# Kernel optimization log

Measured on AMD Instinct MI355X. Metric: run time of the kernel, lower is better.

Reference implementation:

```python
import jax, jax.numpy as jnp
import numpy as np

ALPHA = 0.02
NEG = -9e15

def lrelu(x):
    return jnp.where(x >= 0, x, ALPHA * x)

def layer_norm(x, eps=1e-5):
    m = jnp.mean(x, axis=-1, keepdims=True)
    v = jnp.var(x, axis=-1, keepdims=True)
    return (x - m) * jax.lax.rsqrt(v + eps)

def setup_inputs() -> dict:
    key = jax.random.key(0)
    ks = jax.random.split(key, 10)
    B, N, F_IN, D = 8, 2048, 10, 128
    h = jax.random.normal(ks[0], (B, N, F_IN), jnp.float32)
    adj = jax.random.randint(ks[1], (B, N, N), 0, 2, jnp.int32)
    s = 0.1
    return {
        "h": h,
        "adj": adj,
        "W1": jax.random.normal(ks[2], (D, F_IN), jnp.float32) * s,
        "b1": jax.random.normal(ks[3], (D,), jnp.float32) * s,
        "Wg": jax.random.normal(ks[4], (D, D), jnp.float32) * s,
        "bg": jax.random.normal(ks[5], (D,), jnp.float32) * s,
        "a1": jax.random.normal(ks[6], (D,), jnp.float32) * s,
        "a2": jax.random.normal(ks[7], (D,), jnp.float32) * s,
        "W2": jax.random.normal(ks[8], (2, D), jnp.float32) * s,
        "b2": jax.random.normal(ks[9], (2,), jnp.float32) * s,
    }

def reference(h, adj, W1, b1, Wg, bg, a1, a2, W2, b2):
    # fc1 + layernorm + leakyrelu
    x = h @ W1.T + b1                      # [B,N,128]
    x = lrelu(layer_norm(x))
    # GAT layer
    Wh = x @ Wg.T + bg                     # [B,N,128]
    e1 = Wh @ a1                           # [B,N]
    e2 = Wh @ a2                           # [B,N]
    e = lrelu(e1[:, :, None] + e2[:, None, :])  # [B,N,N]
    e = jnp.where(adj != 0, e, NEG)
    attn = jax.nn.softmax(e, axis=2)
    hp = jnp.einsum('bij,bjd->bid', attn, Wh)    # [B,N,128]
    hp = lrelu(layer_norm(hp))
    # global max pool over nodes
    pooled = jnp.max(hp, axis=1)           # [B,128]
    out = pooled @ W2.T + b2               # [B,2]
    return jax.nn.log_softmax(out, axis=-1)
```

## Files before the change

### kernel.cpp

```cpp
#include <hip/hip_runtime.h>

#define B 8
#define N 2048
#define FIN 10
#define D 128
#define ALPHA 0.02f
#define BR 32
#define TI 32
#define JC 64
#define NCH (N / JC)
#define NBLK_ATTN ((N / TI) * B)

#define WHT_OFF 0
#define ADJ_OFF 49152
#define E2_OFF  73728
#define ARENA_SZ 74496

typedef short bf8 __attribute__((ext_vector_type(8)));
typedef float f32x4 __attribute__((ext_vector_type(4)));

__device__ __forceinline__ float lrelu(float x) { return x >= 0.f ? x : ALPHA * x; }

__device__ __forceinline__ short f2b(float f) {
    unsigned u = __float_as_uint(f);
    return (short)((u + 0x7fffu + ((u >> 16) & 1u)) >> 16);
}

__device__ __forceinline__ float b2f(short s) {
    return __uint_as_float(((unsigned)(unsigned short)s) << 16);
}

__device__ __forceinline__ unsigned enc_key(float v) {
    unsigned b = __float_as_uint(v);
    return (b & 0x80000000u) ? ~b : (b | 0x80000000u);
}
__device__ __forceinline__ float dec_key(unsigned k) {
    unsigned b = (k & 0x80000000u) ? (k & 0x7fffffffu) : ~k;
    return __uint_as_float(b);
}

__device__ __forceinline__ void dma16(const void* g, void* l) {
    __builtin_amdgcn_global_load_lds(
        (const __attribute__((address_space(1))) void*)g,
        (__attribute__((address_space(3))) void*)l, 16, 0, 0);
}
__device__ __forceinline__ void dma4(const void* g, void* l) {
    __builtin_amdgcn_global_load_lds(
        (const __attribute__((address_space(1))) void*)g,
        (__attribute__((address_space(3))) void*)l, 4, 0, 0);
}

__global__ __launch_bounds__(256) void k_proj(
    const float* __restrict__ h, const float* __restrict__ W1, const float* __restrict__ b1,
    const float* __restrict__ Wg, const float* __restrict__ bg,
    const float* __restrict__ a1, const float* __restrict__ a2,
    unsigned short* __restrict__ WhT, float* __restrict__ e1g, float* __restrict__ e2g,
    unsigned* __restrict__ pooled, unsigned* __restrict__ cnt)
{
    __shared__ __align__(16) short xep_lds[32 * 136];
    __shared__ __align__(16) short wg_lds[D * 136];
    __shared__ float W1_lds[D * 11];
    __shared__ float h_lds[BR * FIN];
    __shared__ float ep1[2][BR], ep2[2][BR];

    const int t = threadIdx.x;
    const int r0 = blockIdx.x * BR;
    const int bb = r0 >> 11;
    const int jloc = r0 & (N - 1);

    if (blockIdx.x < B && t < D) pooled[blockIdx.x * D + t] = 0u;
    if (blockIdx.x == 0 && t == 128) *cnt = 0u;

    for (int idx = t; idx < D * FIN; idx += 256)
        W1_lds[(idx / FIN) * 11 + (idx % FIN)] = W1[idx];
    for (int idx = t; idx < BR * FIN; idx += 256)
        h_lds[idx] = h[(size_t)r0 * FIN + idx];
    __syncthreads();

    {
        const int dr = t >> 4;
        const int j8 = t & 15;
        #pragma unroll
        for (int pass = 0; pass < 8; pass++) {
            int dd = pass * 16 + dr;
            float4 f0 = *(const float4*)&Wg[dd * D + j8 * 8];
            float4 f1 = *(const float4*)&Wg[dd * D + j8 * 8 + 4];
            bf8 v;
            v[0] = f2b(f0.x); v[1] = f2b(f0.y); v[2] = f2b(f0.z); v[3] = f2b(f0.w);
            v[4] = f2b(f1.x); v[5] = f2b(f1.y); v[6] = f2b(f1.z); v[7] = f2b(f1.w);
            *(bf8*)&wg_lds[dd * 136 + j8 * 8] = v;
        }
    }

    const int w = t >> 6, lane = t & 63;
    {
        float b1v0 = b1[lane], b1v1 = b1[lane + 64];
        for (int i = 0; i < 8; i++) {
            int r = w * 8 + i;
            float s0 = b1v0, s1 = b1v1;
            const float* hr = &h_lds[r * FIN];
            #pragma unroll
            for (int k = 0; k < FIN; k++) {
                float hv = hr[k];
                s0 += hv * W1_lds[lane * 11 + k];
                s1 += hv * W1_lds[(lane + 64) * 11 + k];
            }
            float sm = s0 + s1, sq = s0 * s0 + s1 * s1;
            #pragma unroll
            for (int m = 1; m <= 32; m <<= 1) { sm += __shfl_xor(sm, m); sq += __shfl_xor(sq, m); }
            float mean = sm * (1.f / D);
            float var  = sq * (1.f / D) - mean * mean;
            float rs = rsqrtf(var + 1e-5f);
            xep_lds[r * 136 + lane]      = f2b(lrelu((s0 - mean) * rs));
            xep_lds[r * 136 + lane + 64] = f2b(lrelu((s1 - mean) * rs));
        }
    }
    __syncthreads();

    const int l15 = lane & 15, q = lane >> 4;
    const int mw = w & 1, np = w >> 1;
    f32x4 acc[4];
    #pragma unroll
    for (int nt = 0; nt < 4; nt++)
        #pragma unroll
        for (int r = 0; r < 4; r++) acc[nt][r] = 0.f;

    #pragma unroll
    for (int ks = 0; ks < 4; ks++) {
        bf8 av = *(const bf8*)&xep_lds[(mw * 16 + l15) * 136 + ks * 32 + q * 8];
        #pragma unroll
        for (int nt = 0; nt < 4; nt++) {
            bf8 bv = *(const bf8*)&wg_lds[((np * 4 + nt) * 16 + l15) * 136 + ks * 32 + q * 8];
            acc[nt] = __builtin_amdgcn_mfma_f32_16x16x32_bf16(av, bv, acc[nt], 0, 0, 0);
        }
    }

    float e1p[4] = {0.f, 0.f, 0.f, 0.f}, e2p[4] = {0.f, 0.f, 0.f, 0.f};
    #pragma unroll
    for (int nt = 0; nt < 4; nt++) {
        int col = (np * 4 + nt) * 16 + l15;
        float bgv = bg[col], a1v = a1[col], a2v = a2[col];
        #pragma unroll
        for (int r = 0; r < 4; r++) {
            float v = acc[nt][r] + bgv;
            acc[nt][r] = v;
            e1p[r] += v * a1v;
            e2p[r] += v * a2v;
        }
    }
    #pragma unroll
    for (int m = 1; m <= 8; m <<= 1) {
        #pragma unroll
        for (int r = 0; r < 4; r++) { e1p[r] += __shfl_xor(e1p[r], m); e2p[r] += __shfl_xor(e2p[r], m); }
    }
    if (l15 == 0) {
        #pragma unroll
        for (int r = 0; r < 4; r++) {
            ep1[np][mw * 16 + q * 4 + r] = e1p[r];
            ep2[np][mw * 16 + q * 4 + r] = e2p[r];
        }
    }
    __syncthreads();
    if (t < BR) {
        e1g[r0 + t] = ep1[0][t] + ep1[1][t];
        e2g[r0 + t] = ep2[0][t] + ep2[1][t];
    }
    #pragma unroll
    for (int nt = 0; nt < 4; nt++) {
        int col = (np * 4 + nt) * 16 + l15;
        #pragma unroll
        for (int r = 0; r < 4; r++)
            xep_lds[col * 36 + mw * 16 + q * 4 + r] = f2b(acc[nt][r]);
    }
    __syncthreads();
    {
        const int col = t >> 1, jh = (t & 1) * 16;
        unsigned short* dst = WhT + ((size_t)(bb * D + col)) * N + jloc + jh;
        #pragma unroll
        for (int i2 = 0; i2 < 4; i2++)
            *(uint2*)(dst + i2 * 4) = *(const uint2*)&xep_lds[col * 36 + jh + i2 * 4];
    }
}

__global__ __launch_bounds__(512, 4) void k_attn(
    const int* __restrict__ adj, const unsigned short* __restrict__ WhT,
    const float* __restrict__ e1g, const float* __restrict__ e2g,
    unsigned* __restrict__ pooled, unsigned* __restrict__ cnt,
    const float* __restrict__ W2, const float* __restrict__ b2,
    float* __restrict__ out)
{
    __shared__ __align__(16) char arena[ARENA_SZ];
    __shared__ float lp[8][16];
    __shared__ unsigned maxd[D];
    __shared__ int finalflag;

    const int t = threadIdx.x;
    const int b = blockIdx.y;
    const int i0 = blockIdx.x * TI;

    const int w = t >> 6, lane = t & 63;
    const int l15 = lane & 15, q = lane >> 4;

    const int ib  = w >> 2;
    const int g   = w & 3;
    const int ksw = g & 1;
    const int par = g >> 1;
    const int prow = ib * 16 + l15;

    if (t < D) maxd[t] = 0u;

    const float e1v = e1g[b * N + i0 + prow];
    const unsigned short* WhTb = WhT + (size_t)b * D * N;
    const int* adjb = adj + ((size_t)b * N + i0) * N;
    const float* e2b = e2g + (size_t)b * N;

    f32x4 acc[8];
    #pragma unroll
    for (int db = 0; db < 8; db++)
        #pragma unroll
        for (int r = 0; r < 4; r++) acc[db][r] = 0.f;
    float ls = 0.f;

    auto stage = [&](int jcn, int buf) {
        #pragma unroll
        for (int p = 0; p < 2; p++) {
            int x = p * 8192 + w * 1024 + lane * 16;
            int rowx = x >> 7;
            int scol = (x & 127) ^ ((rowx & 7) << 4);
            dma16((const char*)WhTb + (size_t)rowx * (N * 2) + jcn * (JC * 2) + scol,
                  arena + WHT_OFF + buf * 16384 + x);
        }
        {
            int y = w * 1024 + lane * 16;
            int rowy = y >> 8;
            int scola = (y & 255) ^ ((rowy & 7) << 4);
            dma16((const char*)adjb + (size_t)rowy * (N * 4) + jcn * (JC * 4) + scola,
                  arena + ADJ_OFF + buf * 8192 + y);
        }
        dma4((const char*)e2b + jcn * (JC * 4) + lane * 4,
             arena + E2_OFF + buf * 256 + lane * 4);
    };

    stage(0, 0);

    int cur = 0, nxt = 1;
    for (int jc = 0; jc < NCH; jc++) {
        const int jn = (jc + 1 < NCH) ? jc + 1 : 0;
        stage(jn, nxt);

        asm volatile("s_waitcnt vmcnt(4) lgkmcnt(0)" ::: "memory");
        __builtin_amdgcn_sched_barrier(0);
        __builtin_amdgcn_s_barrier();

        if ((jc & 1) == par) {
            const char* abase = arena + ADJ_OFF + cur * 8192 + prow * 256;
            const int acol = ksw * 128 + q * 32;
            const int sw = (prow & 7) << 4;
            int4 av0 = *(const int4*)(abase + (acol ^ sw));
            int4 av1 = *(const int4*)(abase + ((acol + 16) ^ sw));
            const char* ebase = arena + E2_OFF + cur * 256 + ksw * 128 + q * 32;
            float4 ev0 = *(const float4*)ebase;
            float4 ev1 = *(const float4*)(ebase + 16);

            bf8 pa;
            pa[0] = f2b(av0.x ? __expf(lrelu(e1v + ev0.x)) : 0.f);
            pa[1] = f2b(av0.y ? __expf(lrelu(e1v + ev0.y)) : 0.f);
            pa[2] = f2b(av0.z ? __expf(lrelu(e1v + ev0.z)) : 0.f);
            pa[3] = f2b(av0.w ? __expf(lrelu(e1v + ev0.w)) : 0.f);
            pa[4] = f2b(av1.x ? __expf(lrelu(e1v + ev1.x)) : 0.f);
            pa[5] = f2b(av1.y ? __expf(lrelu(e1v + ev1.y)) : 0.f);
            pa[6] = f2b(av1.z ? __expf(lrelu(e1v + ev1.z)) : 0.f);
            pa[7] = f2b(av1.w ? __expf(lrelu(e1v + ev1.w)) : 0.f);
            ls += b2f(pa[0]) + b2f(pa[1]) + b2f(pa[2]) + b2f(pa[3])
                + b2f(pa[4]) + b2f(pa[5]) + b2f(pa[6]) + b2f(pa[7]);

            __builtin_amdgcn_s_setprio(1);
            #pragma unroll
            for (int db = 0; db < 8; db++) {
                int brow = db * 16 + l15;
                const bf8* bp = (const bf8*)(arena + WHT_OFF + cur * 16384
                                 + brow * 128
                                 + ((ksw * 64 + q * 16) ^ ((brow & 7) << 4)));
                acc[db] = __builtin_amdgcn_mfma_f32_16x16x32_bf16(*bp, pa, acc[db], 0, 0, 0);
            }
            __builtin_amdgcn_s_setprio(0);
        }

        cur = nxt;
        nxt = (nxt + 1 == 3) ? 0 : nxt + 1;
    }

    asm volatile("s_waitcnt vmcnt(0) lgkmcnt(0)" ::: "memory");
    __syncthreads();

    ls += __shfl_xor(ls, 16);
    ls += __shfl_xor(ls, 32);
    if (lane < 16) lp[w][lane] = ls;

    {
        float* obuf = (float*)arena;
        float* orow = obuf + w * (16 * 132) + l15 * 132;
        #pragma unroll
        for (int db = 0; db < 8; db++)
            *(f32x4*)(orow + db * 16 + q * 4) = acc[db];
    }
    __syncthreads();

    {
        const float* obuf = (const float*)arena;
        const int ri = t >> 4;
        const int c  = t & 15;
        const int ibt = ri >> 4, rloc = ri & 15;
        const int dbase = c * 8;
        float lsum = lp[ibt * 4 + 0][rloc] + lp[ibt * 4 + 1][rloc]
                   + lp[ibt * 4 + 2][rloc] + lp[ibt * 4 + 3][rloc];
        float rinv = 1.f / lsum;
        float o[8];
        #pragma unroll
        for (int k = 0; k < 8; k += 4) {
            float4 s0 = *(const float4*)(obuf + (ibt * 4 + 0) * 2112 + rloc * 132 + dbase + k);
            float4 s1 = *(const float4*)(obuf + (ibt * 4 + 1) * 2112 + rloc * 132 + dbase + k);
            float4 s2 = *(const float4*)(obuf + (ibt * 4 + 2) * 2112 + rloc * 132 + dbase + k);
            float4 s3 = *(const float4*)(obuf + (ibt * 4 + 3) * 2112 + rloc * 132 + dbase + k);
            o[k + 0] = (s0.x + s1.x + s2.x + s3.x) * rinv;
            o[k + 1] = (s0.y + s1.y + s2.y + s3.y) * rinv;
            o[k + 2] = (s0.z + s1.z + s2.z + s3.z) * rinv;
            o[k + 3] = (s0.w + s1.w + s2.w + s3.w) * rinv;
        }
        float sm = 0.f, sq = 0.f;
        #pragma unroll
        for (int k = 0; k < 8; k++) { sm += o[k]; sq += o[k] * o[k]; }
        #pragma unroll
        for (int m = 1; m <= 8; m <<= 1) { sm += __shfl_xor(sm, m); sq += __shfl_xor(sq, m); }
        float mean = sm * (1.f / D);
        float var  = sq * (1.f / D) - mean * mean;
        float rs = rsqrtf(var + 1e-5f);
        #pragma unroll
        for (int k = 0; k < 8; k++) {
            float v = lrelu((o[k] - mean) * rs);
            atomicMax(&maxd[dbase + k], enc_key(v));
        }
    }
    __syncthreads();
    if (t < D) atomicMax(&pooled[b * D + t], maxd[t]);
    __syncthreads();

    if (t == 0) {
        __threadfence();
        unsigned old = atomicAdd(cnt, 1u);
        finalflag = (old == NBLK_ATTN - 1) ? 1 : 0;
    }
    __syncthreads();
    if (finalflag && t < 256) {
        const int fb = t >> 5;
        const int fq = t & 31;
        float s0 = 0.f, s1 = 0.f;
        #pragma unroll
        for (int m = 0; m < 4; m++) {
            int dd = fq + 32 * m;
            unsigned key = __hip_atomic_load(&pooled[fb * D + dd], __ATOMIC_RELAXED,
                                             __HIP_MEMORY_SCOPE_AGENT);
            float v = dec_key(key);
            s0 += v * W2[dd];
            s1 += v * W2[D + dd];
        }
        #pragma unroll
        for (int m = 1; m <= 16; m <<= 1) { s0 += __shfl_xor(s0, m); s1 += __shfl_xor(s1, m); }
        if (fq == 0) {
            float o0 = s0 + b2[0], o1 = s1 + b2[1];
            float mxv = fmaxf(o0, o1);
            float ls2 = logf(__expf(o0 - mxv) + __expf(o1 - mxv));
            out[fb * 2 + 0] = o0 - mxv - ls2;
            out[fb * 2 + 1] = o1 - mxv - ls2;
        }
    }
}

extern "C" void kernel_launch(void* const* d_in, const int* in_sizes, int n_in,
                              void* d_out, int out_size, void* d_ws, size_t ws_size,
                              hipStream_t stream) {
    const float* h   = (const float*)d_in[0];
    const int*   adj = (const int*)d_in[1];
    const float* W1  = (const float*)d_in[2];
    const float* b1  = (const float*)d_in[3];
    const float* Wg  = (const float*)d_in[4];
    const float* bg  = (const float*)d_in[5];
    const float* a1  = (const float*)d_in[6];
    const float* a2  = (const float*)d_in[7];
    const float* W2  = (const float*)d_in[8];
    const float* b2  = (const float*)d_in[9];
    float* out = (float*)d_out;

    unsigned short* WhT = (unsigned short*)d_ws;
    float* e1g = (float*)((char*)d_ws + (size_t)B * D * N * 2);
    float* e2g = e1g + (size_t)B * N;
    unsigned* pooled = (unsigned*)(e2g + (size_t)B * N);
    unsigned* cnt = pooled + (size_t)B * D;

    k_proj<<<(B * N) / BR, 256, 0, stream>>>(h, W1, b1, Wg, bg, a1, a2,
                                             WhT, e1g, e2g, pooled, cnt);
    k_attn<<<dim3(N / TI, B), 512, 0, stream>>>(adj, WhT, e1g, e2g, pooled, cnt,
                                                W2, b2, out);
}
```

Measured before the change: 242.9 us.

## Split attention MFMA work across waves by D-half instead of chunk parity

```diff
diff --git a/kernel.cpp b/kernel.cpp
--- a/kernel.cpp
+++ b/kernel.cpp
@@ -202,9 +202,8 @@
     const int l15 = lane & 15, q = lane >> 4;
 
     const int ib  = w >> 2;
-    const int g   = w & 3;
-    const int ksw = g & 1;
-    const int par = g >> 1;
+    const int ksw = (w >> 1) & 1;
+    const int dh  = w & 1;
     const int prow = ib * 16 + l15;
 
     if (t < D) maxd[t] = 0u;
@@ -214,11 +213,11 @@
     const int* adjb = adj + ((size_t)b * N + i0) * N;
     const float* e2b = e2g + (size_t)b * N;
 
-    f32x4 acc[8];
-    #pragma unroll
-    for (int db = 0; db < 8; db++)
-        #pragma unroll
-        for (int r = 0; r < 4; r++) acc[db][r] = 0.f;
+    f32x4 acc[4];
+    #pragma unroll
+    for (int n = 0; n < 4; n++)
+        #pragma unroll
+        for (int r = 0; r < 4; r++) acc[n][r] = 0.f;
     float ls = 0.f;
 
     auto stage = [&](int jcn, int buf) {
@@ -252,7 +251,7 @@
         __builtin_amdgcn_sched_barrier(0);
         __builtin_amdgcn_s_barrier();
 
-        if ((jc & 1) == par) {
+        {
             const char* abase = arena + ADJ_OFF + cur * 8192 + prow * 256;
             const int acol = ksw * 128 + q * 32;
             const int sw = (prow & 7) << 4;
@@ -276,12 +275,12 @@
 
             __builtin_amdgcn_s_setprio(1);
             #pragma unroll
-            for (int db = 0; db < 8; db++) {
-                int brow = db * 16 + l15;
+            for (int n = 0; n < 4; n++) {
+                int brow = (dh * 4 + n) * 16 + l15;
                 const bf8* bp = (const bf8*)(arena + WHT_OFF + cur * 16384
                                  + brow * 128
                                  + ((ksw * 64 + q * 16) ^ ((brow & 7) << 4)));
-                acc[db] = __builtin_amdgcn_mfma_f32_16x16x32_bf16(*bp, pa, acc[db], 0, 0, 0);
+                acc[n] = __builtin_amdgcn_mfma_f32_16x16x32_bf16(*bp, pa, acc[n], 0, 0, 0);
             }
             __builtin_amdgcn_s_setprio(0);
         }
@@ -301,8 +300,8 @@
         float* obuf = (float*)arena;
         float* orow = obuf + w * (16 * 132) + l15 * 132;
         #pragma unroll
-        for (int db = 0; db < 8; db++)
-            *(f32x4*)(orow + db * 16 + q * 4) = acc[db];
+        for (int n = 0; n < 4; n++)
+            *(f32x4*)(orow + (dh * 4 + n) * 16 + q * 4) = acc[n];
     }
     __syncthreads();
 
@@ -312,20 +311,20 @@
         const int c  = t & 15;
         const int ibt = ri >> 4, rloc = ri & 15;
         const int dbase = c * 8;
-        float lsum = lp[ibt * 4 + 0][rloc] + lp[ibt * 4 + 1][rloc]
-                   + lp[ibt * 4 + 2][rloc] + lp[ibt * 4 + 3][rloc];
+        const int dhc = c >> 3;
+        const int s0i = ibt * 4 + 0 + dhc;
+        const int s1i = ibt * 4 + 2 + dhc;
+        float lsum = lp[ibt * 4 + 0][rloc] + lp[ibt * 4 + 2][rloc];
         float rinv = 1.f / lsum;
         float o[8];
         #pragma unroll
         for (int k = 0; k < 8; k += 4) {
-            float4 s0 = *(const float4*)(obuf + (ibt * 4 + 0) * 2112 + rloc * 132 + dbase + k);
-            float4 s1 = *(const float4*)(obuf + (ibt * 4 + 1) * 2112 + rloc * 132 + dbase + k);
-            float4 s2 = *(const float4*)(obuf + (ibt * 4 + 2) * 2112 + rloc * 132 + dbase + k);
-            float4 s3 = *(const float4*)(obuf + (ibt * 4 + 3) * 2112 + rloc * 132 + dbase + k);
-            o[k + 0] = (s0.x + s1.x + s2.x + s3.x) * rinv;
-            o[k + 1] = (s0.y + s1.y + s2.y + s3.y) * rinv;
-            o[k + 2] = (s0.z + s1.z + s2.z + s3.z) * rinv;
-            o[k + 3] = (s0.w + s1.w + s2.w + s3.w) * rinv;
+            float4 s0 = *(const float4*)(obuf + s0i * 2112 + rloc * 132 + dbase + k);
+            float4 s1 = *(const float4*)(obuf + s1i * 2112 + rloc * 132 + dbase + k);
+            o[k + 0] = (s0.x + s1.x) * rinv;
+            o[k + 1] = (s0.y + s1.y) * rinv;
+            o[k + 2] = (s0.z + s1.z) * rinv;
+            o[k + 3] = (s0.w + s1.w) * rinv;
         }
         float sm = 0.f, sq = 0.f;
         #pragma unroll
```

Measured after the change: 247.3 us. No clear change (+1.8%).
